# Optimization experiments

Measured on AMD Instinct MI355X. Metric: run time of the kernel, lower is better.

The kernel has to match this reference:

```python
import jax, jax.numpy as jnp
import numpy as np

H = 16
E = 2048
LAT = E // 4
D = E // H          # 128
R = D // 2          # 64 (rotary dim)
B, S = 2, 2048

def _lin(x, W, b):
    return x @ W.T + b

def _rope_cos_sin(seq_len):
    inv_freq = 1.0 / (10000.0 ** (jnp.arange(0, R, 2, dtype=jnp.float32) / R))  # (R/2,)
    t = jnp.arange(seq_len, dtype=jnp.float32)
    freqs = jnp.outer(t, inv_freq)                 # (S, R/2)
    emb = jnp.concatenate([freqs, freqs], axis=-1) # (S, R)
    return jnp.cos(emb), jnp.sin(emb)

def _rotate_half(x):
    x1, x2 = x[..., : R // 2], x[..., R // 2 :]
    return jnp.concatenate([-x2, x1], axis=-1)

def _apply_rope(x, cos, sin):
    # x: (B, S, H, R); cos/sin: (S, R)
    c = cos[None, :, None, :]
    s = sin[None, :, None, :]
    return x * c + _rotate_half(x) * s

def setup_inputs() -> dict:
    key = jax.random.key(0)
    ks = jax.random.split(key, 20)
    def w(k, o, i):
        return jax.random.normal(k, (o, i), dtype=jnp.float32) * 0.02
    def bvec(k, o):
        return jax.random.normal(k, (o,), dtype=jnp.float32) * 0.02
    return {
        "x": jax.random.normal(ks[0], (B, S, E), dtype=jnp.float32),
        "Wkv_d": w(ks[1], LAT, E), "bkv_d": bvec(ks[2], LAT),
        "Wq_d": w(ks[3], LAT, E), "bq_d": bvec(ks[4], LAT),
        "Wk_u": w(ks[5], E // 2, LAT), "bk_u": bvec(ks[6], E // 2),
        "Wq_u": w(ks[7], E // 2, LAT), "bq_u": bvec(ks[8], E // 2),
        "Wv_u": w(ks[9], E, LAT), "bv_u": bvec(ks[10], E),
        "Wrk": w(ks[11], E // 2, E), "brk": bvec(ks[12], E // 2),
        "Wrq": w(ks[13], E // 2, LAT), "brq": bvec(ks[14], E // 2),
        "Wo": w(ks[15], E, E), "bo": bvec(ks[16], E),
    }

def reference(x, Wkv_d, bkv_d, Wq_d, bq_d, Wk_u, bk_u, Wq_u, bq_u,
              Wv_u, bv_u, Wrk, brk, Wrq, brq, Wo, bo):
    Bn, Sn, _ = x.shape
    kv_d = _lin(x, Wkv_d, bkv_d)                      # (B,S,LAT)
    q_d = _lin(x, Wq_d, bq_d)                         # (B,S,LAT)
    k1 = _lin(kv_d, Wk_u, bk_u).reshape(Bn, Sn, H, R)
    q1 = _lin(q_d, Wq_u, bq_u).reshape(Bn, Sn, H, R)
    v = _lin(kv_d, Wv_u, bv_u).reshape(Bn, Sn, H, D)
    kr = _lin(x, Wrk, brk).reshape(Bn, Sn, H, R)
    qr = _lin(q_d, Wrq, brq).reshape(Bn, Sn, H, R)
    cos, sin = _rope_cos_sin(Sn)
    qr = _apply_rope(qr, cos, sin)
    kr = _apply_rope(kr, cos, sin)
    k = jnp.concatenate([k1, kr], axis=-1)            # (B,S,H,D)
    q = jnp.concatenate([q1, qr], axis=-1)
    scale = 1.0 / np.sqrt(D)
    attn = jnp.einsum("bqhd,bkhd->bhqk", q, k) * scale
    attn = jax.nn.softmax(attn, axis=-1)
    out = jnp.einsum("bhqk,bkhd->bqhd", attn, v).reshape(Bn, Sn, E)
    return _lin(out, Wo, bo)
```

## Files before the change

kernel.cpp:

```cpp
#include <hip/hip_runtime.h>
#include <cmath>

typedef unsigned short ushort_t;
typedef unsigned int u32;
typedef __attribute__((ext_vector_type(8))) __bf16 bf16x8;
typedef __attribute__((ext_vector_type(4))) float f32x4;

#define Hh 16
#define Ss 2048
#define SCALE 0.08838834764831845f

__device__ __forceinline__ ushort_t f2bf(float f) {
  union { float f; unsigned u; } c; c.f = f;
  unsigned u = c.u;
  return (ushort_t)((u + 0x7FFFu + ((u >> 16) & 1u)) >> 16);
}
__device__ __forceinline__ float bf2f(ushort_t h) {
  union { unsigned u; float f; } c; c.u = ((unsigned)h) << 16;
  return c.f;
}
__device__ __forceinline__ u32 cvt_pk_bf16(float lo, float hi) {
  u32 r;
  asm volatile("v_cvt_pk_bf16_f32 %0, %1, %2" : "=v"(r) : "v"(lo), "v"(hi));
  return r;
}

__device__ __forceinline__ void gload_lds16(const ushort_t* g, ushort_t* l) {
  __builtin_amdgcn_global_load_lds(
      (const __attribute__((address_space(1))) u32*)g,
      (__attribute__((address_space(3))) u32*)l, 16, 0, 0);
}

struct SrcPtrs { const float* p[9]; };

__global__ __launch_bounds__(256) void convert_all_kernel(SrcPtrs sp,
    ushort_t* __restrict__ x_bf, ushort_t* __restrict__ wbuf) {
  const int cum[9] = {8192, 9216, 10240, 12288, 12800, 13824, 14336, 14848, 18944};
  const int dsto[9] = {0, 0, 1048576, 2097152, 4194304, 4718592, 5767168, 6291456, 6815744};
  const int bid = blockIdx.x;
  int s = 0;
  #pragma unroll
  for (int i = 0; i < 8; ++i) s += (bid >= cum[i]);
  const int lb = bid - (s == 0 ? 0 : cum[s - 1]);
  const float* src = sp.p[s] + (size_t)lb * 1024;
  ushort_t* dst = (s == 0 ? x_bf : wbuf + dsto[s]) + (size_t)lb * 1024;
  const int i = threadIdx.x * 4;
  float4 v = *(const float4*)&src[i];
  ushort4 o;
  o.x = f2bf(v.x); o.y = f2bf(v.y); o.z = f2bf(v.z); o.w = f2bf(v.w);
  *(ushort4*)&dst[i] = o;
}

template<int MODE, typename OUTT>
__global__ __launch_bounds__(256) void gemm_bf16(
    const ushort_t* __restrict__ A, const ushort_t* __restrict__ W,
    const float* __restrict__ bias, OUTT* __restrict__ C0,
    ushort_t* __restrict__ C1, ushort_t* __restrict__ C2, int K)
{
  __shared__ ushort_t As[128][64];
  __shared__ ushort_t Bs[128][64];
  const int tid = threadIdx.x;
  const int lane = tid & 63;
  const int w = tid >> 6;
  const int wr = w >> 1, wc = w & 1;
  const int l15 = lane & 15, lhi = lane >> 4;
  const int m0 = blockIdx.y * 128, n0 = blockIdx.x * 128;

  if constexpr (MODE == 5) { if (blockIdx.x >= 24) A += 2097152; }

  const int srow_base = w * 8 + (lane >> 3);
  const int scol = (lane & 7) * 8;

  f32x4 acc[4][4];
  #pragma unroll
  for (int i = 0; i < 4; ++i)
    #pragma unroll
    for (int j = 0; j < 4; ++j)
      acc[i][j] = (f32x4){0.f, 0.f, 0.f, 0.f};

  for (int k0 = 0; k0 < K; k0 += 64) {
    __syncthreads();
    #pragma unroll
    for (int q = 0; q < 4; ++q) {
      const int row = q * 32 + srow_base;
      gload_lds16(&A[(size_t)(m0 + row) * K + k0 + scol], &As[q * 32 + w * 8][0]);
      gload_lds16(&W[(size_t)(n0 + row) * K + k0 + scol], &Bs[q * 32 + w * 8][0]);
    }
    __syncthreads();
    #pragma unroll
    for (int dk = 0; dk < 2; ++dk) {
      bf16x8 af[4], bfr[4];
      #pragma unroll
      for (int i = 0; i < 4; ++i)
        af[i] = *(const bf16x8*)&As[wr * 64 + i * 16 + l15][dk * 32 + lhi * 8];
      #pragma unroll
      for (int j = 0; j < 4; ++j)
        bfr[j] = *(const bf16x8*)&Bs[wc * 64 + j * 16 + l15][dk * 32 + lhi * 8];
      #pragma unroll
      for (int i = 0; i < 4; ++i)
        #pragma unroll
        for (int j = 0; j < 4; ++j)
          acc[i][j] = __builtin_amdgcn_mfma_f32_16x16x32_bf16(af[i], bfr[j], acc[i][j], 0, 0, 0);
    }
  }

  #pragma unroll
  for (int i = 0; i < 4; ++i) {
    #pragma unroll
    for (int j = 0; j < 4; ++j) {
      const int n = n0 + wc * 64 + j * 16 + l15;
      const float bz = bias[n];
      #pragma unroll
      for (int r = 0; r < 4; ++r) {
        const int m = m0 + wr * 64 + i * 16 + lhi * 4 + r;
        const float v = acc[i][j][r] + bz;
        if constexpr (MODE == 0) {
          C0[(size_t)m * 2048 + n] = v;
        } else if constexpr (MODE == 2) {
          if (n < 1024)
            C0[(size_t)(n >> 9) * 2097152 + (size_t)m * 512 + (n & 511)] = (OUTT)f2bf(v);
          else {
            const int np = n - 1024;
            C1[(size_t)m * 2048 + (np >> 6) * 128 + (np & 63)] = f2bf(v);
          }
        } else {
          if (n < 1024) {
            C0[(size_t)m * 2048 + (n >> 6) * 128 + (n & 63)] = (OUTT)f2bf(v);
          } else if (n < 3072) {
            const int np = n - 1024;
            C1[(size_t)(m >> 11) * 4194304 + (size_t)np * 2048 + (m & 2047)] = f2bf(v);
          } else {
            const int np = n - 3072;
            const int col = ((np & 1023) >> 6) * 128 + (np & 63) + ((np >> 10) << 6);
            C2[(size_t)m * 2048 + col] = f2bf(v);
          }
        }
      }
    }
  }
}

__global__ __launch_bounds__(256) void rope_bf16_kernel(ushort_t* __restrict__ q,
                                                        ushort_t* __restrict__ k) {
  const int t = threadIdx.x & 63;
  const int idx = blockIdx.x * 4 + (threadIdx.x >> 6);
  const int s = (idx >> 4) & (Ss - 1);
  ushort_t* base = (t < 32 ? q : k) + (size_t)idx * 128 + 64;
  const int i = t & 31;
  const float invf = expf(-logf(10000.f) * (float)i / 32.f);
  const float fr = (float)s * invf;
  const float cs = cosf(fr), sn = sinf(fr);
  const float x1 = bf2f(base[i]);
  const float x2 = bf2f(base[i + 32]);
  base[i]      = f2bf(x1 * cs - x2 * sn);
  base[i + 32] = f2bf(x2 * cs + x1 * sn);
}

__global__ __launch_bounds__(256) void flash_mfma_kernel(
    const ushort_t* __restrict__ Qb, const ushort_t* __restrict__ Kb,
    const ushort_t* __restrict__ Vt, ushort_t* __restrict__ Oattn)
{
  __shared__ ushort_t Ks[64][136];
  __shared__ ushort_t Vs[128][72];
  __shared__ ushort_t Ps[4][32][72];

  const int tid = threadIdx.x, lane = tid & 63, w = tid >> 6;
  const int l15 = lane & 15, lhi = lane >> 4;
  const int bh = blockIdx.y, b = bh >> 4, h = bh & 15;
  const int q0 = blockIdx.x * 128 + w * 32;

  bf16x8 qf[2][4];
  #pragma unroll
  for (int mi = 0; mi < 2; ++mi) {
    const size_t qrow = (size_t)b * Ss + q0 + mi * 16 + l15;
    const ushort_t* qp = Qb + (qrow * Hh + h) * 128;
    #pragma unroll
    for (int dk = 0; dk < 4; ++dk)
      qf[mi][dk] = *(const bf16x8*)(qp + dk * 32 + lhi * 8);
  }

  f32x4 o[2][8];
  #pragma unroll
  for (int mi = 0; mi < 2; ++mi)
    #pragma unroll
    for (int dn = 0; dn < 8; ++dn) o[mi][dn] = (f32x4){0.f, 0.f, 0.f, 0.f};
  float lsum[2] = {0.f, 0.f};

  const size_t kbase_g = (size_t)b * Ss * 2048 + (size_t)h * 128;
  const size_t vbase_g = (size_t)bh * 128 * Ss;

  bf16x8 kv[4], vv[4];
  #pragma unroll
  for (int p = 0; p < 4; ++p) {
    const int idx = p * 256 + tid;
    kv[p] = *(const bf16x8*)&Kb[kbase_g + (size_t)(idx >> 4) * 2048 + (idx & 15) * 8];
    vv[p] = *(const bf16x8*)&Vt[vbase_g + (size_t)(idx >> 3) * Ss + (idx & 7) * 8];
  }

  for (int t = 0; t < Ss / 64; ++t) {
    __syncthreads();
    #pragma unroll
    for (int p = 0; p < 4; ++p) {
      const int idx = p * 256 + tid;
      *(bf16x8*)&Ks[idx >> 4][(idx & 15) * 8] = kv[p];
      *(bf16x8*)&Vs[idx >> 3][(idx & 7) * 8] = vv[p];
    }
    __syncthreads();

    if (t + 1 < Ss / 64) {
      const int s1 = (t + 1) * 64;
      #pragma unroll
      for (int p = 0; p < 4; ++p) {
        const int idx = p * 256 + tid;
        kv[p] = *(const bf16x8*)&Kb[kbase_g + (size_t)(s1 + (idx >> 4)) * 2048 + (idx & 15) * 8];
        vv[p] = *(const bf16x8*)&Vt[vbase_g + (size_t)(idx >> 3) * Ss + s1 + (idx & 7) * 8];
      }
    }

    f32x4 s[2][4];
    #pragma unroll
    for (int mi = 0; mi < 2; ++mi)
      #pragma unroll
      for (int jc = 0; jc < 4; ++jc) s[mi][jc] = (f32x4){0.f, 0.f, 0.f, 0.f};
    #pragma unroll
    for (int jc = 0; jc < 4; ++jc)
      #pragma unroll
      for (int dk = 0; dk < 4; ++dk) {
        bf16x8 ak = *(const bf16x8*)&Ks[jc * 16 + l15][dk * 32 + lhi * 8];
        s[0][jc] = __builtin_amdgcn_mfma_f32_16x16x32_bf16(ak, qf[0][dk], s[0][jc], 0, 0, 0);
        s[1][jc] = __builtin_amdgcn_mfma_f32_16x16x32_bf16(ak, qf[1][dk], s[1][jc], 0, 0, 0);
      }

    #pragma unroll
    for (int mi = 0; mi < 2; ++mi)
      #pragma unroll
      for (int jc = 0; jc < 4; ++jc) {
        const float p0 = __expf(s[mi][jc][0] * SCALE);
        const float p1 = __expf(s[mi][jc][1] * SCALE);
        const float p2 = __expf(s[mi][jc][2] * SCALE);
        const float p3 = __expf(s[mi][jc][3] * SCALE);
        lsum[mi] += (p0 + p1) + (p2 + p3);
        const u32 d0 = cvt_pk_bf16(p0, p1);
        const u32 d1 = cvt_pk_bf16(p2, p3);
        *(uint2*)&Ps[w][mi * 16 + l15][jc * 16 + lhi * 4] = make_uint2(d0, d1);
      }

    #pragma unroll
    for (int kc = 0; kc < 2; ++kc) {
      bf16x8 ap0 = *(const bf16x8*)&Ps[w][l15][kc * 32 + lhi * 8];
      bf16x8 ap1 = *(const bf16x8*)&Ps[w][16 + l15][kc * 32 + lhi * 8];
      #pragma unroll
      for (int dn = 0; dn < 8; ++dn) {
        bf16x8 bv = *(const bf16x8*)&Vs[dn * 16 + l15][kc * 32 + lhi * 8];
        o[0][dn] = __builtin_amdgcn_mfma_f32_16x16x32_bf16(ap0, bv, o[0][dn], 0, 0, 0);
        o[1][dn] = __builtin_amdgcn_mfma_f32_16x16x32_bf16(ap1, bv, o[1][dn], 0, 0, 0);
      }
    }
  }

  #pragma unroll
  for (int mi = 0; mi < 2; ++mi) {
    float v = lsum[mi];
    v += __shfl_xor(v, 16);
    v += __shfl_xor(v, 32);
    lsum[mi] = v;
  }

  #pragma unroll
  for (int mi = 0; mi < 2; ++mi) {
    float inv[4];
    #pragma unroll
    for (int r = 0; r < 4; ++r)
      inv[r] = 1.f / __shfl(lsum[mi], lhi * 4 + r);
    #pragma unroll
    for (int dn = 0; dn < 8; ++dn)
      #pragma unroll
      for (int r = 0; r < 4; ++r) {
        const int row = q0 + mi * 16 + lhi * 4 + r;
        const size_t addr = ((size_t)b * Ss + row) * 2048 + h * 128 + dn * 16 + l15;
        Oattn[addr] = f2bf(o[mi][dn][r] * inv[r]);
      }
  }
}

extern "C" void kernel_launch(void* const* d_in, const int* in_sizes, int n_in,
                              void* d_out, int out_size, void* d_ws, size_t ws_size,
                              hipStream_t stream)
{
  const float* x     = (const float*)d_in[0];
  const float* Wkv_d = (const float*)d_in[1];
  const float* bkv_d = (const float*)d_in[2];
  const float* Wq_d  = (const float*)d_in[3];
  const float* bq_d  = (const float*)d_in[4];
  const float* Wk_u  = (const float*)d_in[5];
  const float* bk_u  = (const float*)d_in[6];
  const float* Wq_u  = (const float*)d_in[7];
  const float* bq_u  = (const float*)d_in[8];
  const float* Wv_u  = (const float*)d_in[9];
  const float* bv_u  = (const float*)d_in[10];
  const float* Wrk   = (const float*)d_in[11];
  const float* brk   = (const float*)d_in[12];
  const float* Wrq   = (const float*)d_in[13];
  const float* brq   = (const float*)d_in[14];
  const float* Wo    = (const float*)d_in[15];
  const float* bo    = (const float*)d_in[16];

  ushort_t* ws = (ushort_t*)d_ws;
  ushort_t* x_bf  = ws;
  ushort_t* kv_d  = ws + 8388608;
  ushort_t* q_d   = ws + 10485760;
  ushort_t* qb    = ws + 12582912;
  ushort_t* kb    = ws + 20971520;
  ushort_t* vt    = ws + 29360128;
  ushort_t* attn  = ws + 37748736;
  ushort_t* wbuf  = ws + 46137344;
  float* bias_x   = (float*)(ws + 57147392);
  float* bias_kvq = (float*)(ws + 57151488);

  SrcPtrs sp;
  sp.p[0] = x;    sp.p[1] = Wkv_d; sp.p[2] = Wq_d; sp.p[3] = Wrk;
  sp.p[4] = Wk_u; sp.p[5] = Wv_u;  sp.p[6] = Wq_u; sp.p[7] = Wrq;
  sp.p[8] = Wo;
  convert_all_kernel<<<dim3(18944), dim3(256), 0, stream>>>(sp, x_bf, wbuf);

  hipMemcpyAsync(bias_x,          bkv_d, 512 * 4,  hipMemcpyDeviceToDevice, stream);
  hipMemcpyAsync(bias_x + 512,    bq_d,  512 * 4,  hipMemcpyDeviceToDevice, stream);
  hipMemcpyAsync(bias_x + 1024,   brk,   1024 * 4, hipMemcpyDeviceToDevice, stream);
  hipMemcpyAsync(bias_kvq,        bk_u,  1024 * 4, hipMemcpyDeviceToDevice, stream);
  hipMemcpyAsync(bias_kvq + 1024, bv_u,  2048 * 4, hipMemcpyDeviceToDevice, stream);
  hipMemcpyAsync(bias_kvq + 3072, bq_u,  1024 * 4, hipMemcpyDeviceToDevice, stream);
  hipMemcpyAsync(bias_kvq + 4096, brq,   1024 * 4, hipMemcpyDeviceToDevice, stream);

  const dim3 blk(256);

  gemm_bf16<2, ushort_t><<<dim3(16, 32), blk, 0, stream>>>(
      x_bf, wbuf, bias_x, kv_d, kb + 64, nullptr, 2048);
  gemm_bf16<5, ushort_t><<<dim3(40, 32), blk, 0, stream>>>(
      kv_d, wbuf + 4194304, bias_kvq, kb, vt, qb, 512);

  rope_bf16_kernel<<<dim3(Ss * Hh * 2 / 4), blk, 0, stream>>>(qb, kb);

  flash_mfma_kernel<<<dim3(Ss / 128, 32), blk, 0, stream>>>(qb, kb, vt, attn);

  gemm_bf16<0, float><<<dim3(16, 32), blk, 0, stream>>>(
      attn, wbuf + 6815744, bo, (float*)d_out, nullptr, nullptr, 2048);
}
```

Baseline: 292.0 us.

## Fuse RoPE into GEMM epilogues and fold bias copies into convert kernel

Applies the rotary embedding inside the epilogues of the projection GEMMs, using a precomputed cos/sin table, and drops the separate rope kernel with its extra read-modify-write pass over q and k. The seven bias hipMemcpyAsync calls are folded into extra blocks of the conversion kernel. A small table-building kernel is added. The rope epilogue issues scattered 2-byte stores, and the table lookup adds global reads per element.

```diff
diff --git a/kernel.cpp b/kernel.cpp
--- a/kernel.cpp
+++ b/kernel.cpp
@@ -31,31 +31,51 @@
       (__attribute__((address_space(3))) u32*)l, 16, 0, 0);
 }
 
-struct SrcPtrs { const float* p[9]; };
+struct SrcPtrs { const float* p[16]; };
 
 __global__ __launch_bounds__(256) void convert_all_kernel(SrcPtrs sp,
-    ushort_t* __restrict__ x_bf, ushort_t* __restrict__ wbuf) {
-  const int cum[9] = {8192, 9216, 10240, 12288, 12800, 13824, 14336, 14848, 18944};
+    ushort_t* __restrict__ x_bf, ushort_t* __restrict__ wbuf,
+    float* __restrict__ biasbuf) {
+  const int cum[16] = {8192, 9216, 10240, 12288, 12800, 13824, 14336, 14848,
+                       18944, 18945, 18946, 18947, 18948, 18950, 18951, 18952};
   const int dsto[9] = {0, 0, 1048576, 2097152, 4194304, 4718592, 5767168, 6291456, 6815744};
+  const int boff[7] = {0, 512, 1024, 2048, 3072, 5120, 6144};
+  const int bsz[7]  = {512, 512, 1024, 1024, 2048, 1024, 1024};
   const int bid = blockIdx.x;
   int s = 0;
   #pragma unroll
-  for (int i = 0; i < 8; ++i) s += (bid >= cum[i]);
+  for (int i = 0; i < 15; ++i) s += (bid >= cum[i]);
   const int lb = bid - (s == 0 ? 0 : cum[s - 1]);
-  const float* src = sp.p[s] + (size_t)lb * 1024;
-  ushort_t* dst = (s == 0 ? x_bf : wbuf + dsto[s]) + (size_t)lb * 1024;
-  const int i = threadIdx.x * 4;
-  float4 v = *(const float4*)&src[i];
-  ushort4 o;
-  o.x = f2bf(v.x); o.y = f2bf(v.y); o.z = f2bf(v.z); o.w = f2bf(v.w);
-  *(ushort4*)&dst[i] = o;
+  const int e = lb * 1024 + threadIdx.x * 4;
+  if (s < 9) {
+    const float* src = sp.p[s] + (size_t)lb * 1024;
+    ushort_t* dst = (s == 0 ? x_bf : wbuf + dsto[s]) + (size_t)lb * 1024;
+    const int i = threadIdx.x * 4;
+    float4 v = *(const float4*)&src[i];
+    ushort4 o;
+    o.x = f2bf(v.x); o.y = f2bf(v.y); o.z = f2bf(v.z); o.w = f2bf(v.w);
+    *(ushort4*)&dst[i] = o;
+  } else {
+    const int k = s - 9;
+    if (e < bsz[k])
+      *(float4*)&biasbuf[boff[k] + e] = *(const float4*)&sp.p[s][e];
+  }
+}
+
+__global__ __launch_bounds__(256) void rope_table_kernel(float2* __restrict__ tb) {
+  const int i = blockIdx.x * 256 + threadIdx.x;
+  const int s = i >> 5, ii = i & 31;
+  const float invf = expf(-logf(10000.f) * (float)ii / 32.f);
+  const float fr = (float)s * invf;
+  tb[i] = make_float2(cosf(fr), sinf(fr));
 }
 
 template<int MODE, typename OUTT>
 __global__ __launch_bounds__(256) void gemm_bf16(
     const ushort_t* __restrict__ A, const ushort_t* __restrict__ W,
     const float* __restrict__ bias, OUTT* __restrict__ C0,
-    ushort_t* __restrict__ C1, ushort_t* __restrict__ C2, int K)
+    ushort_t* __restrict__ C1, ushort_t* __restrict__ C2,
+    const float2* __restrict__ tb, int K)
 {
   __shared__ ushort_t As[128][64];
   __shared__ ushort_t Bs[128][64];
@@ -104,6 +124,47 @@
     }
   }
 
+  const bool rope_region =
+      (MODE == 2 && blockIdx.x >= 8) || (MODE == 5 && blockIdx.x >= 32);
+
+  if (rope_region) {
+    #pragma unroll
+    for (int i = 0; i < 4; ++i) {
+      #pragma unroll
+      for (int p = 0; p < 2; ++p) {
+        const int nA = n0 + wc * 64 + p * 16 + l15;
+        const int nB = nA + 32;
+        const float bzA = bias[nA];
+        const float bzB = bias[nB];
+        int colA, colB;
+        ushort_t* Cb;
+        if constexpr (MODE == 2) {
+          const int npA = nA - 1024;
+          colA = (npA >> 6) * 128 + (npA & 63);
+          colB = colA + 32;
+          Cb = C1;
+        } else {
+          const int npA = nA - 4096;
+          colA = (npA >> 6) * 128 + 64 + (npA & 63);
+          colB = colA + 32;
+          Cb = C2;
+        }
+        const int ii = p * 16 + l15;
+        #pragma unroll
+        for (int r = 0; r < 4; ++r) {
+          const int m = m0 + wr * 64 + i * 16 + lhi * 4 + r;
+          const int s = m & (Ss - 1);
+          const float2 cs = tb[(s << 5) + ii];
+          const float x1 = acc[i][p][r] + bzA;
+          const float x2 = acc[i][p + 2][r] + bzB;
+          Cb[(size_t)m * 2048 + colA] = f2bf(x1 * cs.x - x2 * cs.y);
+          Cb[(size_t)m * 2048 + colB] = f2bf(x2 * cs.x + x1 * cs.y);
+        }
+      }
+    }
+    return;
+  }
+
   #pragma unroll
   for (int i = 0; i < 4; ++i) {
     #pragma unroll
@@ -117,12 +178,7 @@
         if constexpr (MODE == 0) {
           C0[(size_t)m * 2048 + n] = v;
         } else if constexpr (MODE == 2) {
-          if (n < 1024)
-            C0[(size_t)(n >> 9) * 2097152 + (size_t)m * 512 + (n & 511)] = (OUTT)f2bf(v);
-          else {
-            const int np = n - 1024;
-            C1[(size_t)m * 2048 + (np >> 6) * 128 + (np & 63)] = f2bf(v);
-          }
+          C0[(size_t)(n >> 9) * 2097152 + (size_t)m * 512 + (n & 511)] = (OUTT)f2bf(v);
         } else {
           if (n < 1024) {
             C0[(size_t)m * 2048 + (n >> 6) * 128 + (n & 63)] = (OUTT)f2bf(v);
@@ -131,29 +187,12 @@
             C1[(size_t)(m >> 11) * 4194304 + (size_t)np * 2048 + (m & 2047)] = f2bf(v);
           } else {
             const int np = n - 3072;
-            const int col = ((np & 1023) >> 6) * 128 + (np & 63) + ((np >> 10) << 6);
-            C2[(size_t)m * 2048 + col] = f2bf(v);
+            C2[(size_t)m * 2048 + (np >> 6) * 128 + (np & 63)] = f2bf(v);
           }
         }
       }
     }
   }
-}
-
-__global__ __launch_bounds__(256) void rope_bf16_kernel(ushort_t* __restrict__ q,
-                                                        ushort_t* __restrict__ k) {
-  const int t = threadIdx.x & 63;
-  const int idx = blockIdx.x * 4 + (threadIdx.x >> 6);
-  const int s = (idx >> 4) & (Ss - 1);
-  ushort_t* base = (t < 32 ? q : k) + (size_t)idx * 128 + 64;
-  const int i = t & 31;
-  const float invf = expf(-logf(10000.f) * (float)i / 32.f);
-  const float fr = (float)s * invf;
-  const float cs = cosf(fr), sn = sinf(fr);
-  const float x1 = bf2f(base[i]);
-  const float x2 = bf2f(base[i + 32]);
-  base[i]      = f2bf(x1 * cs - x2 * sn);
-  base[i + 32] = f2bf(x2 * cs + x1 * sn);
 }
 
 __global__ __launch_bounds__(256) void flash_mfma_kernel(
@@ -314,34 +353,27 @@
   ushort_t* vt    = ws + 29360128;
   ushort_t* attn  = ws + 37748736;
   ushort_t* wbuf  = ws + 46137344;
-  float* bias_x   = (float*)(ws + 57147392);
-  float* bias_kvq = (float*)(ws + 57151488);
+  float* biasbuf  = (float*)(ws + 57147392);
+  float2* ropetb  = (float2*)(ws + 57161728);
 
   SrcPtrs sp;
-  sp.p[0] = x;    sp.p[1] = Wkv_d; sp.p[2] = Wq_d; sp.p[3] = Wrk;
-  sp.p[4] = Wk_u; sp.p[5] = Wv_u;  sp.p[6] = Wq_u; sp.p[7] = Wrq;
+  sp.p[0] = x;     sp.p[1] = Wkv_d; sp.p[2] = Wq_d;  sp.p[3] = Wrk;
+  sp.p[4] = Wk_u;  sp.p[5] = Wv_u;  sp.p[6] = Wq_u;  sp.p[7] = Wrq;
   sp.p[8] = Wo;
-  convert_all_kernel<<<dim3(18944), dim3(256), 0, stream>>>(sp, x_bf, wbuf);
-
-  hipMemcpyAsync(bias_x,          bkv_d, 512 * 4,  hipMemcpyDeviceToDevice, stream);
-  hipMemcpyAsync(bias_x + 512,    bq_d,  512 * 4,  hipMemcpyDeviceToDevice, stream);
-  hipMemcpyAsync(bias_x + 1024,   brk,   1024 * 4, hipMemcpyDeviceToDevice, stream);
-  hipMemcpyAsync(bias_kvq,        bk_u,  1024 * 4, hipMemcpyDeviceToDevice, stream);
-  hipMemcpyAsync(bias_kvq + 1024, bv_u,  2048 * 4, hipMemcpyDeviceToDevice, stream);
-  hipMemcpyAsync(bias_kvq + 3072, bq_u,  1024 * 4, hipMemcpyDeviceToDevice, stream);
-  hipMemcpyAsync(bias_kvq + 4096, brq,   1024 * 4, hipMemcpyDeviceToDevice, stream);
+  sp.p[9] = bkv_d; sp.p[10] = bq_d; sp.p[11] = brk;  sp.p[12] = bk_u;
+  sp.p[13] = bv_u; sp.p[14] = bq_u; sp.p[15] = brq;
+  convert_all_kernel<<<dim3(18952), dim3(256), 0, stream>>>(sp, x_bf, wbuf, biasbuf);
+  rope_table_kernel<<<dim3(256), dim3(256), 0, stream>>>(ropetb);
 
   const dim3 blk(256);
 
   gemm_bf16<2, ushort_t><<<dim3(16, 32), blk, 0, stream>>>(
-      x_bf, wbuf, bias_x, kv_d, kb + 64, nullptr, 2048);
+      x_bf, wbuf, biasbuf, kv_d, kb + 64, nullptr, ropetb, 2048);
   gemm_bf16<5, ushort_t><<<dim3(40, 32), blk, 0, stream>>>(
-      kv_d, wbuf + 4194304, bias_kvq, kb, vt, qb, 512);
-
-  rope_bf16_kernel<<<dim3(Ss * Hh * 2 / 4), blk, 0, stream>>>(qb, kb);
+      kv_d, wbuf + 4194304, biasbuf + 2048, kb, vt, qb, ropetb, 512);
 
   flash_mfma_kernel<<<dim3(Ss / 128, 32), blk, 0, stream>>>(qb, kb, vt, attn);
 
   gemm_bf16<0, float><<<dim3(16, 32), blk, 0, stream>>>(
-      attn, wbuf + 6815744, bo, (float*)d_out, nullptr, nullptr, 2048);
-}
+      attn, wbuf + 6815744, bo, (float*)d_out, nullptr, nullptr, nullptr, 2048);
+}
```

After: 269.5 us. 7.7% less time.
